# Kernel tuning notes

Hardware: AMD Instinct MI355X
Metric: run time of the kernel (lower is better)

## Reference

```python
import jax, jax.numpy as jnp
import numpy as np
import math

N_HEADS = 12
HEAD_DIM = 64
D_MODEL = 768
BATCH = 2
SEQ = 2048
GRID = 46  # num_patches_per_side


def _rope_1d(x, pos, dim):
    # x: (B,S,H,dim), pos: (S,) int -> rotary embedding along last dim
    inv_freq = 1.0 / (10000.0 ** (jnp.arange(0, dim, 2, dtype=jnp.float32) / dim))  # (dim/2,)
    ang = pos.astype(jnp.float32)[:, None] * inv_freq  # (S, dim/2)
    cos = jnp.concatenate([jnp.cos(ang), jnp.cos(ang)], axis=-1)[None, :, None, :]
    sin = jnp.concatenate([jnp.sin(ang), jnp.sin(ang)], axis=-1)[None, :, None, :]
    x1, x2 = jnp.split(x, 2, axis=-1)
    rot = jnp.concatenate([-x2, x1], axis=-1)
    return x * cos.astype(x.dtype) + rot * sin.astype(x.dtype)


def _rope_2d(x, row_ids, col_ids):
    # 2D RoPE: first half of head_dim rotated by row position, second half by column position
    half = x.shape[-1] // 2
    xr = _rope_1d(x[..., :half], row_ids, half)
    xc = _rope_1d(x[..., half:], col_ids, half)
    return jnp.concatenate([xr, xc], axis=-1)


def setup_inputs() -> dict:
    key = jax.random.key(0)
    ks = jax.random.split(key, 7)
    scale = 1.0 / math.sqrt(D_MODEL)
    return {
        "x": jax.random.normal(ks[0], (BATCH, SEQ, D_MODEL), dtype=jnp.float32),
        "row_ids": jax.random.randint(ks[1], (SEQ,), 0, GRID),
        "col_ids": jax.random.randint(ks[2], (SEQ,), 0, GRID),
        "Wq": jax.random.normal(ks[3], (D_MODEL, D_MODEL), dtype=jnp.float32) * scale,
        "Wk": jax.random.normal(ks[4], (D_MODEL, D_MODEL), dtype=jnp.float32) * scale,
        "Wv": jax.random.normal(ks[5], (D_MODEL, D_MODEL), dtype=jnp.float32) * scale,
        "Wo": jax.random.normal(ks[6], (D_MODEL, D_MODEL), dtype=jnp.float32) * scale,
    }


def reference(x, row_ids, col_ids, Wq, Wk, Wv, Wo):
    B, S, _ = x.shape
    # projections (nn.Linear: y = x @ W.T)
    q = (x @ Wq.T).reshape(B, S, N_HEADS, HEAD_DIM)
    k = (x @ Wk.T).reshape(B, S, N_HEADS, HEAD_DIM)
    v = (x @ Wv.T).reshape(B, S, N_HEADS, HEAD_DIM)
    q = _rope_2d(q, row_ids, col_ids)
    k = _rope_2d(k, row_ids, col_ids)
    # (B,H,S,D)
    q = q.transpose(0, 2, 1, 3)
    k = k.transpose(0, 2, 1, 3)
    v = v.transpose(0, 2, 1, 3)
    scale = 1.0 / math.sqrt(HEAD_DIM)
    scores = jnp.einsum('bhqd,bhkd->bhqk', q, k) * scale  # (B,H,S,S)
    causal = jnp.triu(jnp.ones((S, S), dtype=bool), k=1)
    scores = jnp.where(causal, -jnp.inf, scores)
    attn = jax.nn.softmax(scores, axis=-1)
    out = jnp.einsum('bhqk,bhkd->bhqd', attn, v)
    out = out.transpose(0, 2, 1, 3).reshape(B, S, D_MODEL)
    return out @ Wo.T
```

## Files before the change

### kernel.cpp

```cpp
#include <hip/hip_runtime.h>
#include <stdint.h>
#include <stddef.h>

#define DEV __device__ __forceinline__

typedef unsigned short u16;
typedef __attribute__((ext_vector_type(8))) __bf16 bf16x8;
typedef __attribute__((ext_vector_type(4))) float f32x4;
typedef __attribute__((ext_vector_type(8))) unsigned short u16x8;
typedef __attribute__((ext_vector_type(4))) unsigned short u16x4;

DEV u16 f2bf(float f) {
  uint32_t u = __builtin_bit_cast(uint32_t, f);
  u += 0x7fffu + ((u >> 16) & 1u);
  return (u16)(u >> 16);
}
DEV float bf2f(u16 h) {
  uint32_t u = ((uint32_t)h) << 16;
  return __builtin_bit_cast(float, u);
}
DEV f32x4 mfma16(bf16x8 a, bf16x8 b, f32x4 c) {
  return __builtin_amdgcn_mfma_f32_16x16x32_bf16(a, b, c, 0, 0, 0);
}
DEV void ld_lds16(const void* g, void* l) {
  __builtin_amdgcn_global_load_lds((const __attribute__((address_space(1))) void*)g,
                                   (__attribute__((address_space(3))) void*)l, 16, 0, 0);
}

__global__ __launch_bounds__(256) void k_cvt_all(const float* __restrict__ x,
                                                 const float* __restrict__ wq,
                                                 const float* __restrict__ wk,
                                                 const float* __restrict__ wv,
                                                 const float* __restrict__ wo,
                                                 u16* __restrict__ dx,
                                                 u16* __restrict__ dqkv,
                                                 u16* __restrict__ dwo) {
  const int bid = blockIdx.x;
  const float* src;
  u16* dst;
  int off;
  if (bid < 3072) {
    src = x; dst = dx; off = bid;
  } else {
    const int t = bid - 3072;
    const int w = t / 576;
    off = t - w * 576;
    src = (w == 0) ? wq : (w == 1) ? wk : (w == 2) ? wv : wo;
    dst = (w < 3) ? (dqkv + (size_t)w * 589824) : dwo;
  }
  const int i = (off * 256 + threadIdx.x) * 4;
  const float4 f = *(const float4*)(src + i);
  u16x4 o;
  o.x = f2bf(f.x); o.y = f2bf(f.y); o.z = f2bf(f.z); o.w = f2bf(f.w);
  *(u16x4*)(dst + i) = o;
}

template <bool OUT_F32>
__global__ __launch_bounds__(256, 4) void k_gemm64(const u16* __restrict__ A,
                                                   const u16* __restrict__ B,
                                                   void* __restrict__ Cv,
                                                   int N, int K) {
  __shared__ __align__(16) u16 sA[64 * 64];
  __shared__ __align__(16) u16 sB[128 * 64];
  const int tid = threadIdx.x;
  const int lane = tid & 63;
  const int wid = tid >> 6;
  const int col16 = lane & 15, quad = lane >> 4;
  const int rowBase = blockIdx.y * 64;
  const int colBase = blockIdx.x * 128;
  const int seg_r = lane >> 3;
  const int seg_c = lane & 7;

  f32x4 zero; zero[0] = zero[1] = zero[2] = zero[3] = 0.0f;
  f32x4 acc[4][2];
#pragma unroll
  for (int i = 0; i < 4; ++i) { acc[i][0] = zero; acc[i][1] = zero; }

  for (int k0 = 0; k0 < K; k0 += 64) {
#pragma unroll
    for (int c = 0; c < 2; ++c) {
      const int seg = wid * 2 + c;
      ld_lds16(A + (size_t)(rowBase + seg * 8 + seg_r) * K + k0 + seg_c * 8, sA + seg * 512);
    }
#pragma unroll
    for (int c = 0; c < 4; ++c) {
      const int seg = wid * 4 + c;
      ld_lds16(B + (size_t)(colBase + seg * 8 + seg_r) * K + k0 + seg_c * 8, sB + seg * 512);
    }
    __syncthreads();
#pragma unroll
    for (int kk = 0; kk < 2; ++kk) {
      bf16x8 af[4], bfr[2];
#pragma unroll
      for (int t = 0; t < 4; ++t)
        af[t] = *(const bf16x8*)(sA + (t * 16 + col16) * 64 + kk * 32 + quad * 8);
#pragma unroll
      for (int t = 0; t < 2; ++t)
        bfr[t] = *(const bf16x8*)(sB + (wid * 32 + t * 16 + col16) * 64 + kk * 32 + quad * 8);
#pragma unroll
      for (int tm = 0; tm < 4; ++tm)
#pragma unroll
        for (int tn = 0; tn < 2; ++tn)
          acc[tm][tn] = mfma16(af[tm], bfr[tn], acc[tm][tn]);
    }
    __syncthreads();
  }

#pragma unroll
  for (int tm = 0; tm < 4; ++tm)
#pragma unroll
    for (int tn = 0; tn < 2; ++tn)
#pragma unroll
      for (int r = 0; r < 4; ++r) {
        const int row = rowBase + tm * 16 + quad * 4 + r;
        const int col = colBase + wid * 32 + tn * 16 + col16;
        const float v = acc[tm][tn][r];
        if (OUT_F32) ((float*)Cv)[(size_t)row * N + col] = v;
        else         ((u16*)Cv)[(size_t)row * N + col] = f2bf(v);
      }
}

__global__ __launch_bounds__(256, 3) void k_gemm_o(const u16* __restrict__ A,
                                                   const u16* __restrict__ B,
                                                   float* __restrict__ C,
                                                   int N, int K) {
  __shared__ __align__(16) u16 sA[64 * 72];
  __shared__ __align__(16) u16 sB[64 * 72];
  const int tid = threadIdx.x;
  const int lane = tid & 63;
  const int wid = tid >> 6;
  const int col16 = lane & 15, quad = lane >> 4;
  const int wm = wid & 1, wn = wid >> 1;
  const int rowBase = blockIdx.y * 64;
  const int colBase = blockIdx.x * 64;
  const int sr = tid >> 3;
  const int sc8 = (tid & 7) * 8;

  f32x4 zero; zero[0] = zero[1] = zero[2] = zero[3] = 0.0f;
  f32x4 acc[2][2];
  acc[0][0] = zero; acc[0][1] = zero; acc[1][0] = zero; acc[1][1] = zero;

  u16x8 ar[2], br[2];
  auto gload = [&](int k0) {
    ar[0] = *(const u16x8*)(A + (size_t)(rowBase + sr) * K + k0 + sc8);
    ar[1] = *(const u16x8*)(A + (size_t)(rowBase + 32 + sr) * K + k0 + sc8);
    br[0] = *(const u16x8*)(B + (size_t)(colBase + sr) * K + k0 + sc8);
    br[1] = *(const u16x8*)(B + (size_t)(colBase + 32 + sr) * K + k0 + sc8);
  };

  gload(0);
  for (int k0 = 0; k0 < K; k0 += 64) {
    __syncthreads();
    *(u16x8*)&sA[sr * 72 + sc8] = ar[0];
    *(u16x8*)&sA[(32 + sr) * 72 + sc8] = ar[1];
    *(u16x8*)&sB[sr * 72 + sc8] = br[0];
    *(u16x8*)&sB[(32 + sr) * 72 + sc8] = br[1];
    if (k0 + 64 < K) gload(k0 + 64);
    __syncthreads();
#pragma unroll
    for (int kk = 0; kk < 2; ++kk) {
      bf16x8 af[2], bfr[2];
#pragma unroll
      for (int t = 0; t < 2; ++t) {
        af[t]  = *(const bf16x8*)&sA[(wm * 32 + t * 16 + col16) * 72 + kk * 32 + quad * 8];
        bfr[t] = *(const bf16x8*)&sB[(wn * 32 + t * 16 + col16) * 72 + kk * 32 + quad * 8];
      }
#pragma unroll
      for (int tm = 0; tm < 2; ++tm)
#pragma unroll
        for (int tn = 0; tn < 2; ++tn)
          acc[tm][tn] = mfma16(af[tm], bfr[tn], acc[tm][tn]);
    }
  }

#pragma unroll
  for (int tm = 0; tm < 2; ++tm)
#pragma unroll
    for (int tn = 0; tn < 2; ++tn)
#pragma unroll
      for (int r = 0; r < 4; ++r) {
        const int row = rowBase + wm * 32 + tm * 16 + quad * 4 + r;
        const int col = colBase + wn * 32 + tn * 16 + col16;
        C[(size_t)row * N + col] = acc[tm][tn][r];
      }
}

__global__ __launch_bounds__(256) void k_rope_vtrans(const u16* __restrict__ QKV,
                                                     const int* __restrict__ row_ids,
                                                     const int* __restrict__ col_ids,
                                                     u16* __restrict__ Qh,
                                                     u16* __restrict__ Kh,
                                                     u16* __restrict__ Vt) {
  __shared__ __align__(16) u16 tile[64][72];
  if (blockIdx.x < 6144) {
    const int t = blockIdx.x * 256 + threadIdx.x;
    const int p = t & 31;
    const int rest = t >> 5;
    const int h = rest % 12;
    const int bs = rest / 12;
    const int s = bs & 2047;
    const int b = bs >> 11;
    const int f = p & 15;
    const int hs = p >> 4;
    const int pos = hs ? col_ids[s] : row_ids[s];
    const float ang = (float)pos * expf(-(float)f * 0.5756462732485114f);
    float sn, cs;
    sincosf(ang, &sn, &cs);
    const int d1 = hs * 32 + f;
    const int d2 = d1 + 16;
    const size_t ibase = (size_t)bs * 2304 + h * 64;
    const size_t obase = (((size_t)b * 12 + h) * 2048 + s) * 64;
    {
      const float x1 = bf2f(QKV[ibase + d1]);
      const float x2 = bf2f(QKV[ibase + d2]);
      Qh[obase + d1] = f2bf(x1 * cs - x2 * sn);
      Qh[obase + d2] = f2bf(x2 * cs + x1 * sn);
    }
    {
      const float x1 = bf2f(QKV[ibase + 768 + d1]);
      const float x2 = bf2f(QKV[ibase + 768 + d2]);
      Kh[obase + d1] = f2bf(x1 * cs - x2 * sn);
      Kh[obase + d2] = f2bf(x2 * cs + x1 * sn);
    }
  } else {
    const int vb = blockIdx.x - 6144;
    const int s0 = (vb & 31) * 64;
    const int bh = vb >> 5;
    const int b = bh / 12, h = bh % 12;
    const int tid = threadIdx.x;
    const int rl = tid >> 2;
    const int cb = (tid & 3) * 16;
    const u16* src = QKV + ((size_t)b * 2048 + s0 + rl) * 2304 + 1536 + h * 64 + cb;
    const u16x8 v0 = *(const u16x8*)src;
    const u16x8 v1 = *(const u16x8*)(src + 8);
    *(u16x8*)&tile[rl][cb] = v0;
    *(u16x8*)&tile[rl][cb + 8] = v1;
    __syncthreads();
    u16x8 o0, o1;
#pragma unroll
    for (int j = 0; j < 8; ++j) {
      o0[j] = tile[cb + j][rl];
      o1[j] = tile[cb + 8 + j][rl];
    }
    u16* dst = Vt + ((size_t)bh * 64 + rl) * 2048 + s0 + cb;
    *(u16x8*)dst = o0;
    *(u16x8*)(dst + 8) = o1;
  }
}

__global__ __launch_bounds__(128, 2) void k_attn(const u16* __restrict__ Qh,
                                                 const u16* __restrict__ Kh,
                                                 const u16* __restrict__ Vt,
                                                 u16* __restrict__ O) {
  __shared__ __align__(16) u16 sK[2][64 * 72];
  __shared__ __align__(16) u16 sV[2][64 * 72];
  __shared__ __align__(16) u16 sP[2][32 * 72];
  const int tid = threadIdx.x;
  const int lane = tid & 63;
  const int wid = tid >> 6;
  const int col16 = lane & 15;
  const int quad = lane >> 4;
  const int fIdx = blockIdx.x;
  const int b3 = fIdx & 7;
  const int r_ = fIdx >> 3;
  const int g_ = r_ >> 5;
  const int qt = 31 - (r_ & 31);
  const int bh = b3 + 8 * g_;
  const int b = bh / 12, h = bh % 12;
  const int qw = qt * 64 + wid * 32;
  const int nkt = qt + 1;

  const u16* Qb = Qh + (size_t)bh * (2048 * 64);
  const u16* Kb = Kh + (size_t)bh * (2048 * 64);
  const u16* Vb = Vt + (size_t)bh * (64 * 2048);

  const int sr = tid >> 3;
  const int sc8 = (tid & 7) * 8;

  bf16x8 bQ[2][2];
#pragma unroll
  for (int g = 0; g < 2; ++g) {
    const u16* qp = Qb + (size_t)(qw + g * 16 + col16) * 64 + quad * 8;
    bQ[g][0] = *(const bf16x8*)qp;
    bQ[g][1] = *(const bf16x8*)(qp + 32);
  }

  f32x4 zero; zero[0] = zero[1] = zero[2] = zero[3] = 0.0f;
  f32x4 o[2][4];
#pragma unroll
  for (int g = 0; g < 2; ++g)
#pragma unroll
    for (int i = 0; i < 4; ++i) o[g][i] = zero;
  float m_r[2] = {-1e30f, -1e30f}, l_r[2] = {0.0f, 0.0f};

  u16* sPw = &sP[wid][0];

  u16x8 kr[4], vr[4];
  auto gload = [&](int kt) {
#pragma unroll
    for (int i = 0; i < 4; ++i) {
      const int row = sr + i * 16;
      kr[i] = *(const u16x8*)(Kb + (size_t)(kt + row) * 64 + sc8);
      vr[i] = *(const u16x8*)(Vb + (size_t)row * 2048 + kt + sc8);
    }
  };
  auto lwrite = [&](int buf) {
#pragma unroll
    for (int i = 0; i < 4; ++i) {
      const int row = sr + i * 16;
      *(u16x8*)&sK[buf][row * 72 + sc8] = kr[i];
      *(u16x8*)&sV[buf][row * 72 + sc8] = vr[i];
    }
  };

  gload(0);
  lwrite(0);
  if (nkt > 1) gload(64);
  __syncthreads();

  for (int ki = 0; ki < nkt; ++ki) {
    const int buf = ki & 1;
    const int kt = ki * 64;
    if (ki + 1 < nkt) {
      lwrite(buf ^ 1);
      if (ki + 2 < nkt) gload(kt + 128);
    }
    bf16x8 ka0[4], ka1[4];
#pragma unroll
    for (int tn = 0; tn < 4; ++tn) {
      const int base = (tn * 16 + col16) * 72 + quad * 8;
      ka0[tn] = *(const bf16x8*)&sK[buf][base];
      ka1[tn] = *(const bf16x8*)&sK[buf][base + 32];
    }
    f32x4 sc[2][4];
#pragma unroll
    for (int tn = 0; tn < 4; ++tn) {
      sc[0][tn] = mfma16(ka1[tn], bQ[0][1], mfma16(ka0[tn], bQ[0][0], zero));
      sc[1][tn] = mfma16(ka1[tn], bQ[1][1], mfma16(ka0[tn], bQ[1][0], zero));
    }
    bf16x8 va0[4], va1[4];
#pragma unroll
    for (int tn = 0; tn < 4; ++tn) {
      const int base = (tn * 16 + col16) * 72 + quad * 8;
      va0[tn] = *(const bf16x8*)&sV[buf][base];
      va1[tn] = *(const bf16x8*)&sV[buf][base + 32];
    }
#pragma unroll
    for (int g = 0; g < 2; ++g) {
      const int qrow = qw + g * 16 + col16;
      if (kt + 63 > qw + g * 16) {
#pragma unroll
        for (int tn = 0; tn < 4; ++tn)
#pragma unroll
          for (int rr = 0; rr < 4; ++rr) {
            float v = sc[g][tn][rr] * 0.125f;
            if (kt + tn * 16 + quad * 4 + rr > qrow) v = -1e30f;
            sc[g][tn][rr] = v;
          }
      } else {
#pragma unroll
        for (int tn = 0; tn < 4; ++tn)
#pragma unroll
          for (int rr = 0; rr < 4; ++rr) sc[g][tn][rr] *= 0.125f;
      }
      float vm = sc[g][0][0];
#pragma unroll
      for (int tn = 0; tn < 4; ++tn)
#pragma unroll
        for (int rr = 0; rr < 4; ++rr) vm = fmaxf(vm, sc[g][tn][rr]);
      vm = fmaxf(vm, __shfl_xor(vm, 16, 64));
      vm = fmaxf(vm, __shfl_xor(vm, 32, 64));
      const float mn = fmaxf(m_r[g], vm);
      const float alpha = __expf(m_r[g] - mn);
      m_r[g] = mn;
      float rs = 0.0f;
#pragma unroll
      for (int tn = 0; tn < 4; ++tn)
#pragma unroll
        for (int h2 = 0; h2 < 2; ++h2) {
          const float p0 = __expf(sc[g][tn][2 * h2] - mn);
          const float p1 = __expf(sc[g][tn][2 * h2 + 1] - mn);
          rs += p0 + p1;
          const uint32_t w = (uint32_t)f2bf(p0) | ((uint32_t)f2bf(p1) << 16);
          ((uint32_t*)sPw)[(g * 16 + col16) * 36 + tn * 8 + quad * 2 + h2] = w;
        }
      rs += __shfl_xor(rs, 16, 64);
      rs += __shfl_xor(rs, 32, 64);
      l_r[g] = l_r[g] * alpha + rs;
#pragma unroll
      for (int t = 0; t < 4; ++t)
#pragma unroll
        for (int rr = 0; rr < 4; ++rr) o[g][t][rr] *= alpha;
    }
    asm volatile("s_waitcnt lgkmcnt(0)" ::: "memory");
#pragma unroll
    for (int g = 0; g < 2; ++g) {
      const bf16x8 bP0 = *(const bf16x8*)(sPw + (g * 16 + col16) * 72 + quad * 8);
      const bf16x8 bP1 = *(const bf16x8*)(sPw + (g * 16 + col16) * 72 + 32 + quad * 8);
#pragma unroll
      for (int tn = 0; tn < 4; ++tn)
        o[g][tn] = mfma16(va1[tn], bP1, mfma16(va0[tn], bP0, o[g][tn]));
    }
    __syncthreads();
  }

#pragma unroll
  for (int g = 0; g < 2; ++g) {
    const float invl = 1.0f / l_r[g];
    const size_t row = (size_t)b * 2048 + qw + g * 16 + col16;
#pragma unroll
    for (int tn = 0; tn < 4; ++tn)
#pragma unroll
      for (int h2 = 0; h2 < 2; ++h2) {
        const float v0 = o[g][tn][2 * h2] * invl;
        const float v1 = o[g][tn][2 * h2 + 1] * invl;
        const uint32_t w = (uint32_t)f2bf(v0) | ((uint32_t)f2bf(v1) << 16);
        const int col = h * 64 + tn * 16 + quad * 4 + 2 * h2;
        *(uint32_t*)(O + row * 768 + col) = w;
      }
  }
}

extern "C" void kernel_launch(void* const* d_in, const int* in_sizes, int n_in,
                              void* d_out, int out_size, void* d_ws, size_t ws_size,
                              hipStream_t stream) {
  const float* x       = (const float*)d_in[0];
  const int*   row_ids = (const int*)d_in[1];
  const int*   col_ids = (const int*)d_in[2];
  const float* Wq      = (const float*)d_in[3];
  const float* Wk      = (const float*)d_in[4];
  const float* Wv      = (const float*)d_in[5];
  const float* Wo      = (const float*)d_in[6];
  float* out = (float*)d_out;

  uint8_t* w8 = (uint8_t*)d_ws;
  u16* x_bf = (u16*)(w8 + 0);
  u16* wqkv = (u16*)(w8 + 6291456);
  u16* wo   = (u16*)(w8 + 9830400);
  u16* qkv  = (u16*)(w8 + 11010048);
  u16* qh   = (u16*)(w8 + 29884416);
  u16* kh   = (u16*)(w8 + 36175872);
  u16* vt   = (u16*)(w8 + 42467328);
  u16* obuf = (u16*)(w8 + 48758784);

  k_cvt_all<<<5376, 256, 0, stream>>>(x, Wq, Wk, Wv, Wo, x_bf, wqkv, wo);
  k_gemm64<false><<<dim3(18, 64), 256, 0, stream>>>(x_bf, wqkv, (void*)qkv, 2304, 768);
  k_rope_vtrans<<<6912, 256, 0, stream>>>(qkv, row_ids, col_ids, qh, kh, vt);
  k_attn<<<768, 128, 0, stream>>>(qh, kh, vt, obuf);
  k_gemm_o<<<dim3(12, 64), 256, 0, stream>>>(obuf, wo, out, 768, 768);
}
```

Baseline: 205.9 us.

## Split causal attention along KV into chunks with a combine pass; enlarge QKV GEMM tile

Attention is restructured split-KV style. Each query tile's KV range is cut into chunks of up to 8 tiles, giving 1920 blocks of 4 waves (16 query rows per wave) instead of 768 blocks of 2 waves. Partial outputs and per-row max/sum go to a scratch buffer that reuses the qkv region, and a new combine kernel merges them. This is meant to balance the causal triangle across CUs and raise occupancy, at the cost of extra partial traffic, an extra launch and bf16 rounding of partials. Separately, the QKV GEMM tile grows from 64x128 to 128x128 with a 2x2 wave layout for more reuse per load.

```diff
diff --git a/kernel.cpp b/kernel.cpp
--- a/kernel.cpp
+++ b/kernel.cpp
@@ -56,51 +56,49 @@
 }
 
 template <bool OUT_F32>
-__global__ __launch_bounds__(256, 4) void k_gemm64(const u16* __restrict__ A,
-                                                   const u16* __restrict__ B,
-                                                   void* __restrict__ Cv,
-                                                   int N, int K) {
-  __shared__ __align__(16) u16 sA[64 * 64];
+__global__ __launch_bounds__(256) void k_gemm_bt(const u16* __restrict__ A,
+                                                 const u16* __restrict__ B,
+                                                 void* __restrict__ Cv,
+                                                 int N, int K) {
+  __shared__ __align__(16) u16 sA[128 * 64];
   __shared__ __align__(16) u16 sB[128 * 64];
   const int tid = threadIdx.x;
   const int lane = tid & 63;
   const int wid = tid >> 6;
+  const int wm = wid & 1, wn = wid >> 1;
   const int col16 = lane & 15, quad = lane >> 4;
-  const int rowBase = blockIdx.y * 64;
+  const int rowBase = blockIdx.y * 128;
   const int colBase = blockIdx.x * 128;
   const int seg_r = lane >> 3;
   const int seg_c = lane & 7;
 
   f32x4 zero; zero[0] = zero[1] = zero[2] = zero[3] = 0.0f;
-  f32x4 acc[4][2];
-#pragma unroll
-  for (int i = 0; i < 4; ++i) { acc[i][0] = zero; acc[i][1] = zero; }
+  f32x4 acc[4][4];
+#pragma unroll
+  for (int i = 0; i < 4; ++i)
+#pragma unroll
+    for (int j = 0; j < 4; ++j) acc[i][j] = zero;
 
   for (int k0 = 0; k0 < K; k0 += 64) {
-#pragma unroll
-    for (int c = 0; c < 2; ++c) {
-      const int seg = wid * 2 + c;
-      ld_lds16(A + (size_t)(rowBase + seg * 8 + seg_r) * K + k0 + seg_c * 8, sA + seg * 512);
-    }
 #pragma unroll
     for (int c = 0; c < 4; ++c) {
       const int seg = wid * 4 + c;
+      ld_lds16(A + (size_t)(rowBase + seg * 8 + seg_r) * K + k0 + seg_c * 8, sA + seg * 512);
       ld_lds16(B + (size_t)(colBase + seg * 8 + seg_r) * K + k0 + seg_c * 8, sB + seg * 512);
     }
     __syncthreads();
 #pragma unroll
     for (int kk = 0; kk < 2; ++kk) {
-      bf16x8 af[4], bfr[2];
-#pragma unroll
-      for (int t = 0; t < 4; ++t)
-        af[t] = *(const bf16x8*)(sA + (t * 16 + col16) * 64 + kk * 32 + quad * 8);
-#pragma unroll
-      for (int t = 0; t < 2; ++t)
-        bfr[t] = *(const bf16x8*)(sB + (wid * 32 + t * 16 + col16) * 64 + kk * 32 + quad * 8);
+      bf16x8 af[4], bfr[4];
+#pragma unroll
+      for (int t = 0; t < 4; ++t) {
+        af[t]  = *(const bf16x8*)(sA + (wm * 64 + t * 16 + col16) * 64 + kk * 32 + quad * 8);
+        bfr[t] = *(const bf16x8*)(sB + (wn * 64 + t * 16 + col16) * 64 + kk * 32 + quad * 8);
+      }
 #pragma unroll
       for (int tm = 0; tm < 4; ++tm)
 #pragma unroll
-        for (int tn = 0; tn < 2; ++tn)
+        for (int tn = 0; tn < 4; ++tn)
           acc[tm][tn] = mfma16(af[tm], bfr[tn], acc[tm][tn]);
     }
     __syncthreads();
@@ -109,11 +107,11 @@
 #pragma unroll
   for (int tm = 0; tm < 4; ++tm)
 #pragma unroll
-    for (int tn = 0; tn < 2; ++tn)
+    for (int tn = 0; tn < 4; ++tn)
 #pragma unroll
       for (int r = 0; r < 4; ++r) {
-        const int row = rowBase + tm * 16 + quad * 4 + r;
-        const int col = colBase + wid * 32 + tn * 16 + col16;
+        const int row = rowBase + wm * 64 + tm * 16 + quad * 4 + r;
+        const int col = colBase + wn * 64 + tn * 16 + col16;
         const float v = acc[tm][tn][r];
         if (OUT_F32) ((float*)Cv)[(size_t)row * N + col] = v;
         else         ((u16*)Cv)[(size_t)row * N + col] = f2bf(v);
@@ -248,82 +246,79 @@
   }
 }
 
-__global__ __launch_bounds__(128, 2) void k_attn(const u16* __restrict__ Qh,
+__global__ __launch_bounds__(256, 3) void k_attn(const u16* __restrict__ Qh,
                                                  const u16* __restrict__ Kh,
                                                  const u16* __restrict__ Vt,
-                                                 u16* __restrict__ O) {
+                                                 u16* __restrict__ O,
+                                                 u16* __restrict__ Opart,
+                                                 float* __restrict__ ml) {
   __shared__ __align__(16) u16 sK[2][64 * 72];
   __shared__ __align__(16) u16 sV[2][64 * 72];
-  __shared__ __align__(16) u16 sP[2][32 * 72];
+  __shared__ __align__(16) u16 sP[4][16 * 72];
   const int tid = threadIdx.x;
   const int lane = tid & 63;
   const int wid = tid >> 6;
   const int col16 = lane & 15;
   const int quad = lane >> 4;
-  const int fIdx = blockIdx.x;
-  const int b3 = fIdx & 7;
-  const int r_ = fIdx >> 3;
-  const int g_ = r_ >> 5;
-  const int qt = 31 - (r_ & 31);
-  const int bh = b3 + 8 * g_;
+  const int bx = blockIdx.x;
+  const int bh = bx / 80;
+  const int u = bx - bh * 80;
+  int qt, c;
+  if (u < 8)       { qt = u; c = 0; }
+  else if (u < 24) { const int t = u - 8;  qt = 8 + (t >> 1); c = t & 1; }
+  else if (u < 48) { const int t = u - 24; const int q3 = t / 3; qt = 16 + q3; c = t - q3 * 3; }
+  else             { const int t = u - 48; qt = 24 + (t >> 2); c = t & 3; }
+  const int nc = (qt >> 3) + 1;
+  const int tile0 = c * 8;
+  const int tileE = min(tile0 + 8, qt + 1);
+  const int ntiles = tileE - tile0;
   const int b = bh / 12, h = bh % 12;
-  const int qw = qt * 64 + wid * 32;
-  const int nkt = qt + 1;
+  const int qw = qt * 64 + wid * 16;
 
   const u16* Qb = Qh + (size_t)bh * (2048 * 64);
   const u16* Kb = Kh + (size_t)bh * (2048 * 64);
   const u16* Vb = Vt + (size_t)bh * (64 * 2048);
 
+  const bf16x8 bQ0 = *(const bf16x8*)(Qb + (size_t)(qw + col16) * 64 + quad * 8);
+  const bf16x8 bQ1 = *(const bf16x8*)(Qb + (size_t)(qw + col16) * 64 + 32 + quad * 8);
+
+  f32x4 zero; zero[0] = zero[1] = zero[2] = zero[3] = 0.0f;
+  f32x4 o[4];
+#pragma unroll
+  for (int i = 0; i < 4; ++i) o[i] = zero;
+  float m_r = -1e30f, l_r = 0.0f;
+
+  u16* sPw = &sP[wid][0];
+
   const int sr = tid >> 3;
   const int sc8 = (tid & 7) * 8;
-
-  bf16x8 bQ[2][2];
-#pragma unroll
-  for (int g = 0; g < 2; ++g) {
-    const u16* qp = Qb + (size_t)(qw + g * 16 + col16) * 64 + quad * 8;
-    bQ[g][0] = *(const bf16x8*)qp;
-    bQ[g][1] = *(const bf16x8*)(qp + 32);
-  }
-
-  f32x4 zero; zero[0] = zero[1] = zero[2] = zero[3] = 0.0f;
-  f32x4 o[2][4];
-#pragma unroll
-  for (int g = 0; g < 2; ++g)
-#pragma unroll
-    for (int i = 0; i < 4; ++i) o[g][i] = zero;
-  float m_r[2] = {-1e30f, -1e30f}, l_r[2] = {0.0f, 0.0f};
-
-  u16* sPw = &sP[wid][0];
-
-  u16x8 kr[4], vr[4];
+  u16x8 kr[2], vr[2];
   auto gload = [&](int kt) {
 #pragma unroll
-    for (int i = 0; i < 4; ++i) {
-      const int row = sr + i * 16;
-      kr[i] = *(const u16x8*)(Kb + (size_t)(kt + row) * 64 + sc8);
-      vr[i] = *(const u16x8*)(Vb + (size_t)row * 2048 + kt + sc8);
+    for (int i = 0; i < 2; ++i) {
+      kr[i] = *(const u16x8*)(Kb + (size_t)(kt + sr + i * 32) * 64 + sc8);
+      vr[i] = *(const u16x8*)(Vb + (size_t)(sr + i * 32) * 2048 + kt + sc8);
     }
   };
   auto lwrite = [&](int buf) {
 #pragma unroll
-    for (int i = 0; i < 4; ++i) {
-      const int row = sr + i * 16;
-      *(u16x8*)&sK[buf][row * 72 + sc8] = kr[i];
-      *(u16x8*)&sV[buf][row * 72 + sc8] = vr[i];
+    for (int i = 0; i < 2; ++i) {
+      *(u16x8*)&sK[buf][(sr + i * 32) * 72 + sc8] = kr[i];
+      *(u16x8*)&sV[buf][(sr + i * 32) * 72 + sc8] = vr[i];
     }
   };
 
-  gload(0);
+  gload(tile0 * 64);
   lwrite(0);
-  if (nkt > 1) gload(64);
+  if (ntiles > 1) gload((tile0 + 1) * 64);
   __syncthreads();
 
-  for (int ki = 0; ki < nkt; ++ki) {
+  for (int ki = 0; ki < ntiles; ++ki) {
     const int buf = ki & 1;
-    const int kt = ki * 64;
-    if (ki + 1 < nkt) {
+    const int kt = (tile0 + ki) * 64;
+    if (ki + 1 < ntiles) {
       lwrite(buf ^ 1);
-      if (ki + 2 < nkt) gload(kt + 128);
+      if (ki + 2 < ntiles) gload((tile0 + ki + 2) * 64);
     }
     bf16x8 ka0[4], ka1[4];
 #pragma unroll
@@ -332,12 +327,10 @@
       ka0[tn] = *(const bf16x8*)&sK[buf][base];
       ka1[tn] = *(const bf16x8*)&sK[buf][base + 32];
     }
-    f32x4 sc[2][4];
-#pragma unroll
-    for (int tn = 0; tn < 4; ++tn) {
-      sc[0][tn] = mfma16(ka1[tn], bQ[0][1], mfma16(ka0[tn], bQ[0][0], zero));
-      sc[1][tn] = mfma16(ka1[tn], bQ[1][1], mfma16(ka0[tn], bQ[1][0], zero));
-    }
+    f32x4 sc[4];
+#pragma unroll
+    for (int tn = 0; tn < 4; ++tn)
+      sc[tn] = mfma16(ka1[tn], bQ1, mfma16(ka0[tn], bQ0, zero));
     bf16x8 va0[4], va1[4];
 #pragma unroll
     for (int tn = 0; tn < 4; ++tn) {
@@ -345,80 +338,139 @@
       va0[tn] = *(const bf16x8*)&sV[buf][base];
       va1[tn] = *(const bf16x8*)&sV[buf][base + 32];
     }
-#pragma unroll
-    for (int g = 0; g < 2; ++g) {
-      const int qrow = qw + g * 16 + col16;
-      if (kt + 63 > qw + g * 16) {
-#pragma unroll
-        for (int tn = 0; tn < 4; ++tn)
-#pragma unroll
-          for (int rr = 0; rr < 4; ++rr) {
-            float v = sc[g][tn][rr] * 0.125f;
-            if (kt + tn * 16 + quad * 4 + rr > qrow) v = -1e30f;
-            sc[g][tn][rr] = v;
-          }
-      } else {
-#pragma unroll
-        for (int tn = 0; tn < 4; ++tn)
-#pragma unroll
-          for (int rr = 0; rr < 4; ++rr) sc[g][tn][rr] *= 0.125f;
-      }
-      float vm = sc[g][0][0];
+    if (kt + 63 > qw) {
 #pragma unroll
       for (int tn = 0; tn < 4; ++tn)
 #pragma unroll
-        for (int rr = 0; rr < 4; ++rr) vm = fmaxf(vm, sc[g][tn][rr]);
-      vm = fmaxf(vm, __shfl_xor(vm, 16, 64));
-      vm = fmaxf(vm, __shfl_xor(vm, 32, 64));
-      const float mn = fmaxf(m_r[g], vm);
-      const float alpha = __expf(m_r[g] - mn);
-      m_r[g] = mn;
-      float rs = 0.0f;
+        for (int rr = 0; rr < 4; ++rr) {
+          float v = sc[tn][rr] * 0.125f;
+          if (kt + tn * 16 + quad * 4 + rr > qw + col16) v = -1e30f;
+          sc[tn][rr] = v;
+        }
+    } else {
 #pragma unroll
       for (int tn = 0; tn < 4; ++tn)
 #pragma unroll
-        for (int h2 = 0; h2 < 2; ++h2) {
-          const float p0 = __expf(sc[g][tn][2 * h2] - mn);
-          const float p1 = __expf(sc[g][tn][2 * h2 + 1] - mn);
-          rs += p0 + p1;
-          const uint32_t w = (uint32_t)f2bf(p0) | ((uint32_t)f2bf(p1) << 16);
-          ((uint32_t*)sPw)[(g * 16 + col16) * 36 + tn * 8 + quad * 2 + h2] = w;
-        }
-      rs += __shfl_xor(rs, 16, 64);
-      rs += __shfl_xor(rs, 32, 64);
-      l_r[g] = l_r[g] * alpha + rs;
-#pragma unroll
-      for (int t = 0; t < 4; ++t)
-#pragma unroll
-        for (int rr = 0; rr < 4; ++rr) o[g][t][rr] *= alpha;
-    }
+        for (int rr = 0; rr < 4; ++rr) sc[tn][rr] *= 0.125f;
+    }
+    float vm = sc[0][0];
+#pragma unroll
+    for (int tn = 0; tn < 4; ++tn)
+#pragma unroll
+      for (int rr = 0; rr < 4; ++rr) vm = fmaxf(vm, sc[tn][rr]);
+    vm = fmaxf(vm, __shfl_xor(vm, 16, 64));
+    vm = fmaxf(vm, __shfl_xor(vm, 32, 64));
+    const float mn = fmaxf(m_r, vm);
+    const float alpha = __expf(m_r - mn);
+    m_r = mn;
+    float rs = 0.0f;
+#pragma unroll
+    for (int tn = 0; tn < 4; ++tn)
+#pragma unroll
+      for (int h2 = 0; h2 < 2; ++h2) {
+        const float p0 = __expf(sc[tn][2 * h2] - mn);
+        const float p1 = __expf(sc[tn][2 * h2 + 1] - mn);
+        rs += p0 + p1;
+        const uint32_t w = (uint32_t)f2bf(p0) | ((uint32_t)f2bf(p1) << 16);
+        ((uint32_t*)sPw)[col16 * 36 + tn * 8 + quad * 2 + h2] = w;
+      }
+    rs += __shfl_xor(rs, 16, 64);
+    rs += __shfl_xor(rs, 32, 64);
+    l_r = l_r * alpha + rs;
+#pragma unroll
+    for (int t = 0; t < 4; ++t)
+#pragma unroll
+      for (int rr = 0; rr < 4; ++rr) o[t][rr] *= alpha;
     asm volatile("s_waitcnt lgkmcnt(0)" ::: "memory");
-#pragma unroll
-    for (int g = 0; g < 2; ++g) {
-      const bf16x8 bP0 = *(const bf16x8*)(sPw + (g * 16 + col16) * 72 + quad * 8);
-      const bf16x8 bP1 = *(const bf16x8*)(sPw + (g * 16 + col16) * 72 + 32 + quad * 8);
-#pragma unroll
-      for (int tn = 0; tn < 4; ++tn)
-        o[g][tn] = mfma16(va1[tn], bP1, mfma16(va0[tn], bP0, o[g][tn]));
-    }
+    const bf16x8 bP0 = *(const bf16x8*)(sPw + col16 * 72 + quad * 8);
+    const bf16x8 bP1 = *(const bf16x8*)(sPw + col16 * 72 + 32 + quad * 8);
+#pragma unroll
+    for (int tn = 0; tn < 4; ++tn)
+      o[tn] = mfma16(va1[tn], bP1, mfma16(va0[tn], bP0, o[tn]));
     __syncthreads();
   }
 
-#pragma unroll
-  for (int g = 0; g < 2; ++g) {
-    const float invl = 1.0f / l_r[g];
-    const size_t row = (size_t)b * 2048 + qw + g * 16 + col16;
+  if (nc == 1) {
+    const float invl = 1.0f / l_r;
+    const size_t row = (size_t)b * 2048 + qw + col16;
 #pragma unroll
     for (int tn = 0; tn < 4; ++tn)
 #pragma unroll
       for (int h2 = 0; h2 < 2; ++h2) {
-        const float v0 = o[g][tn][2 * h2] * invl;
-        const float v1 = o[g][tn][2 * h2 + 1] * invl;
+        const float v0 = o[tn][2 * h2] * invl;
+        const float v1 = o[tn][2 * h2 + 1] * invl;
         const uint32_t w = (uint32_t)f2bf(v0) | ((uint32_t)f2bf(v1) << 16);
         const int col = h * 64 + tn * 16 + quad * 4 + 2 * h2;
         *(uint32_t*)(O + row * 768 + col) = w;
       }
-  }
+  } else {
+    u16* op = Opart + (size_t)bx * 4096 + (wid * 16 + col16) * 64;
+#pragma unroll
+    for (int tn = 0; tn < 4; ++tn)
+#pragma unroll
+      for (int h2 = 0; h2 < 2; ++h2) {
+        const uint32_t w = (uint32_t)f2bf(o[tn][2 * h2]) | ((uint32_t)f2bf(o[tn][2 * h2 + 1]) << 16);
+        *(uint32_t*)(op + tn * 16 + quad * 4 + 2 * h2) = w;
+      }
+    if (quad == 0) {
+      float* mlp = ml + (size_t)bx * 128;
+      mlp[wid * 16 + col16] = m_r;
+      mlp[64 + wid * 16 + col16] = l_r;
+    }
+  }
+}
+
+__global__ __launch_bounds__(256) void k_combine(const u16* __restrict__ Opart,
+                                                 const float* __restrict__ ml,
+                                                 u16* __restrict__ O) {
+  const int bx = blockIdx.x;
+  const int bh = bx / 24;
+  const int qt = 8 + (bx - bh * 24);
+  const int b = bh / 12, h = bh % 12;
+  const int nc = (qt >> 3) + 1;
+  const int prefix = (qt < 16) ? (8 + 2 * (qt - 8))
+                   : (qt < 24) ? (24 + 3 * (qt - 16))
+                               : (48 + 4 * (qt - 24));
+  const int slot0 = bh * 80 + prefix;
+  const int tid = threadIdx.x;
+  const int r = tid >> 2;
+  const int d0 = (tid & 3) * 16;
+
+  float m_i[4], w_i[4];
+  float M = -1e30f;
+  for (int i = 0; i < nc; ++i) {
+    m_i[i] = ml[(size_t)(slot0 + i) * 128 + r];
+    M = fmaxf(M, m_i[i]);
+  }
+  float l = 0.0f;
+  for (int i = 0; i < nc; ++i) {
+    w_i[i] = __expf(m_i[i] - M);
+    l += w_i[i] * ml[(size_t)(slot0 + i) * 128 + 64 + r];
+  }
+  const float invl = 1.0f / l;
+
+  float a[16];
+#pragma unroll
+  for (int j = 0; j < 16; ++j) a[j] = 0.0f;
+  for (int i = 0; i < nc; ++i) {
+    const u16* op = Opart + (size_t)(slot0 + i) * 4096 + r * 64 + d0;
+    const u16x8 v0 = *(const u16x8*)op;
+    const u16x8 v1 = *(const u16x8*)(op + 8);
+#pragma unroll
+    for (int j = 0; j < 8; ++j) {
+      a[j] += w_i[i] * bf2f(v0[j]);
+      a[8 + j] += w_i[i] * bf2f(v1[j]);
+    }
+  }
+  u16x8 o0, o1;
+#pragma unroll
+  for (int j = 0; j < 8; ++j) {
+    o0[j] = f2bf(a[j] * invl);
+    o1[j] = f2bf(a[8 + j] * invl);
+  }
+  u16* dst = O + (size_t)(b * 2048 + qt * 64 + r) * 768 + h * 64 + d0;
+  *(u16x8*)dst = o0;
+  *(u16x8*)(dst + 8) = o1;
 }
 
 extern "C" void kernel_launch(void* const* d_in, const int* in_sizes, int n_in,
@@ -442,10 +494,13 @@
   u16* kh   = (u16*)(w8 + 36175872);
   u16* vt   = (u16*)(w8 + 42467328);
   u16* obuf = (u16*)(w8 + 48758784);
+  u16*   opart = (u16*)(w8 + 11010048);
+  float* mlbuf = (float*)(w8 + 11010048 + 15728640);
 
   k_cvt_all<<<5376, 256, 0, stream>>>(x, Wq, Wk, Wv, Wo, x_bf, wqkv, wo);
-  k_gemm64<false><<<dim3(18, 64), 256, 0, stream>>>(x_bf, wqkv, (void*)qkv, 2304, 768);
+  k_gemm_bt<false><<<dim3(18, 32), 256, 0, stream>>>(x_bf, wqkv, (void*)qkv, 2304, 768);
   k_rope_vtrans<<<6912, 256, 0, stream>>>(qkv, row_ids, col_ids, qh, kh, vt);
-  k_attn<<<768, 128, 0, stream>>>(qh, kh, vt, obuf);
+  k_attn<<<1920, 256, 0, stream>>>(qh, kh, vt, obuf, opart, mlbuf);
+  k_combine<<<576, 256, 0, stream>>>(opart, mlbuf, obuf);
   k_gemm_o<<<dim3(12, 64), 256, 0, stream>>>(obuf, wo, out, 768, 768);
 }
```

Result: faster. 190.0 us (-7.7%).
